# Performance work log

Measured on AMD Instinct MI355X. Metric: run time of the kernel, lower is better.

The kernel has to match this reference:

```python
import jax, jax.numpy as jnp
import numpy as np

B, D = 8, 256
MEM, CW, R, K, KL = 131072, 64, 4, 4, 4
C = R * K + 2 * KL + 1  # 25 visible cells
DELTA = 0.005
EPS = 1e-6
TIMESTEP = 1.0  # first step after reset


def _gather(x, idx):
    # x: (b,m) or (b,m,w); idx: (b,k)
    if x.ndim == 2:
        return jnp.take_along_axis(x, idx, axis=1)
    e = jnp.broadcast_to(idx[:, :, None], idx.shape + (x.shape[-1],))
    return jnp.take_along_axis(x, e, axis=1)


def _fwd(xi, memory, visible_memory, link_matrix, rev_link_matrix, precedence,
         read_weights, write_weights, usage,
         W_rq, b_rq, W_wv, b_wv, W_ig, b_ig, W_wg, b_wg,
         read_positions):
    b = xi.shape[0]
    bidx = jnp.arange(b)[:, None]

    # interface transforms (independent linears)
    read_query = (xi @ W_rq + b_rq).reshape(b, R, CW)      # (b,r,w)
    write_vector = (xi @ W_wv + b_wv).reshape(b, 1, CW)    # (b,1,w)
    ig = jax.nn.sigmoid(xi @ W_ig + b_ig)                  # (b,c)
    wg = jax.nn.sigmoid(xi @ W_wg + b_wg)                  # (b,1)

    # ------------------ write ------------------
    rw_vis = _gather(read_weights, read_positions)         # (b,c)
    ww_vis = _gather(write_weights, read_positions)        # (b,c)

    # usage update + least-used indicator over visible cells
    u = (rw_vis + ww_vis > DELTA).astype(memory.dtype)
    rel = _gather(usage, read_positions)
    I_min = (rel == jnp.min(rel, axis=-1, keepdims=True)).astype(memory.dtype)
    rel_new = (TIMESTEP - rel) * u + rel * (1.0 - u)
    usage = usage.at[bidx, read_positions].set(rel_new)

    # interpolated write weights over visible cells
    ww_new = wg * (ig * rw_vis + (1.0 - ig) * I_min)       # (b,c)
    write_weights = write_weights.at[bidx, read_positions].set(ww_new)

    # erase + write into visible memory, scatter back into sparse memory
    visible_memory = visible_memory * (1.0 - I_min[:, :, None]) + ww_new[:, :, None] * write_vector
    memory = memory.at[bidx, read_positions].set(visible_memory)

    # link matrix / reverse link matrix update
    trp = read_positions[:, R * K:R * K + 2 * KL]          # temporal positions (b,2KL)
    Ieye = jnp.eye(MEM, 2 * KL, dtype=memory.dtype)[None]  # eye(m,k) mask as in torch code
    prec_dense = jnp.zeros_like(write_weights).at[bidx, trp].set(precedence)  # (b,m)
    tww = _gather(write_weights, trp)                      # (b,2KL)
    link_matrix = ((1.0 - write_weights[:, :, None]) * link_matrix
                   + write_weights[:, :, None] * precedence[:, None, :]) * Ieye
    rev_link_matrix = ((1.0 - tww[:, None, :]) * rev_link_matrix
                       + tww[:, None, :] * prec_dense[:, :, None]) * Ieye

    # precedence update and least-used cell (argmin usage)
    precedence = (1.0 - jnp.sum(tww, axis=-1, keepdims=True)) * precedence + tww
    least_used = jax.lax.top_k(-usage, 1)[1]               # (b,1)

    # ------------------ read ------------------
    trw = _gather(read_weights, trp)                       # (b,2KL)
    fwd_w = jnp.einsum('bmk,bk->bm', link_matrix, trw)     # forward weighting
    bwd_w = jnp.einsum('bmk,bk->bm', rev_link_matrix, trw) # backward weighting

    # exact L2 k-NN over full memory (dense surrogate for the FAISS search)
    mem_sq = jnp.sum(memory * memory, axis=-1)             # (b,m)
    dots = jnp.einsum('brw,bmw->brm', read_query, memory)  # (b,r,m)
    knn = jax.lax.top_k(2.0 * dots - mem_sq[:, None, :], K)[1].reshape(b, R * K)

    fp = jax.lax.top_k(fwd_w, KL)[1]
    bp = jax.lax.top_k(bwd_w, KL)[1]
    lum = jnp.full((b, 1), C + 1, dtype=knn.dtype)         # timestep <= mem_size branch
    max_length = least_used[0, 0]                          # mem_limit_reached == False
    positions = jnp.clip(
        jnp.concatenate([knn, fp.astype(knn.dtype), bp.astype(knn.dtype), lum], axis=1),
        0, max_length)                                     # (b,c)

    visible = _gather(memory, positions)                   # (b,c,w)
    kq = read_query / (jnp.linalg.norm(read_query, axis=-1, keepdims=True) + EPS)
    vn = visible / (jnp.linalg.norm(visible, axis=-1, keepdims=True) + EPS)
    sim = jnp.einsum('brw,bcw->brc', kq, vn)               # cosine similarity
    rw_c = jax.nn.softmax(sim, axis=-1)                    # (b,r,c)
    read_vectors = jnp.einsum('brc,bcw->brw', rw_c, visible)
    return read_vectors


def setup_inputs() -> dict:
    key = jax.random.key(0)
    ks = jax.random.split(key, 16)
    inp = {}
    inp['xi'] = jax.random.normal(ks[0], (B, D), jnp.float32)
    inp['memory'] = jax.random.normal(ks[1], (B, MEM, CW), jnp.float32)
    inp['visible_memory'] = jax.random.normal(ks[2], (B, C, CW), jnp.float32)
    inp['link_matrix'] = 0.1 * jax.random.uniform(ks[3], (B, MEM, 2 * KL), jnp.float32)
    inp['rev_link_matrix'] = 0.1 * jax.random.uniform(ks[4], (B, MEM, 2 * KL), jnp.float32)
    inp['precedence'] = 0.1 * jax.random.uniform(ks[5], (B, 2 * KL), jnp.float32)
    inp['read_weights'] = 0.01 * jax.random.uniform(ks[6], (B, MEM), jnp.float32)
    inp['write_weights'] = 0.01 * jax.random.uniform(ks[7], (B, MEM), jnp.float32)
    usage = 0.5 + 0.5 * jax.random.uniform(ks[8], (B, MEM), jnp.float32)
    inp['usage'] = usage.at[:, MEM - 1].set(0.0)  # argmin lands at m-1 so the clamp is a no-op
    inp['least_used_mem'] = jnp.full((B, 1), MEM // 2, jnp.int32)
    inp['read_positions'] = jax.random.randint(ks[9], (B, C), 0, MEM)

    def lin(k, fi, fo):
        s = (6.0 / fi) ** 0.5  # kaiming-uniform-like
        return jax.random.uniform(k, (fi, fo), jnp.float32, -s, s)
    inp['W_rq'] = lin(ks[10], D, R * CW); inp['b_rq'] = jnp.zeros((R * CW,), jnp.float32)
    inp['W_wv'] = lin(ks[11], D, CW);     inp['b_wv'] = jnp.zeros((CW,), jnp.float32)
    inp['W_ig'] = lin(ks[12], D, C);      inp['b_ig'] = jnp.zeros((C,), jnp.float32)
    inp['W_wg'] = lin(ks[13], D, 1);      inp['b_wg'] = jnp.zeros((1,), jnp.float32)
    return inp


def reference(xi, memory, visible_memory, link_matrix, rev_link_matrix, precedence,
              read_weights, write_weights, usage, least_used_mem, read_positions,
              W_rq, b_rq, W_wv, b_wv, W_ig, b_ig, W_wg, b_wg):
    # least_used_mem is overwritten inside write() (argmin of updated usage) before use
    return _fwd(xi, memory, visible_memory, link_matrix, rev_link_matrix, precedence,
                read_weights, write_weights, usage,
                W_rq, b_rq, W_wv, b_wv, W_ig, b_ig, W_wg, b_wg,
                read_positions)
```

## Files before the change

### kernel.cpp

```cpp
#include <hip/hip_runtime.h>
#include <math.h>

#define BN 8
#define DDIM 256
#define MEMN 131072
#define CWN 64
#define RN 4
#define CN 25
#define DELTA_C 0.005f
#define EPS_C 1e-6f
#define RPB 1024
#define NBLK (MEMN / RPB)
#define NEG_INF (-3.402823466e38f)
#define IMAX 0x7fffffff
#define UPD_STRIDE 32


__device__ inline void wave_reduce_max(float& v, int& i, int& t) {
#pragma unroll
  for (int off = 32; off; off >>= 1) {
    float ov = __shfl_down(v, off);
    int oi = __shfl_down(i, off);
    int ot = __shfl_down(t, off);
    if (ov > v || (ov == v && oi < i)) { v = ov; i = oi; t = ot; }
  }
}

__device__ inline void block_argmax256(int tid, float v, int i, int t,
                                       float& rv, int& ri, int& rt) {
  __shared__ float sv[4];
  __shared__ int si[4], st[4];
  __shared__ float bv;
  __shared__ int bi, bt;
  wave_reduce_max(v, i, t);
  if ((tid & 63) == 0) { int w = tid >> 6; sv[w] = v; si[w] = i; st[w] = t; }
  __syncthreads();
  if (tid == 0) {
    float xv = sv[0]; int xi = si[0], xt = st[0];
#pragma unroll
    for (int w = 1; w < 4; w++)
      if (sv[w] > xv || (sv[w] == xv && si[w] < xi)) { xv = sv[w]; xi = si[w]; xt = st[w]; }
    bv = xv; bi = xi; bt = xt;
  }
  __syncthreads();
  rv = bv; ri = bi; rt = bt;
  __syncthreads();
}

__device__ inline void top4_of8(const float* v8, int* out4) {
  float val[12]; int idx[12]; bool used[12];
#pragma unroll
  for (int i = 0; i < 12; i++) { val[i] = (i < 8) ? v8[i] : 0.f; idx[i] = i; used[i] = false; }
  for (int r = 0; r < 4; r++) {
    int best = -1;
    for (int i = 0; i < 12; i++) {
      if (used[i]) continue;
      if (best < 0 || val[i] > val[best]) best = i;
    }
    used[best] = true;
    out4[r] = idx[best];
  }
}

__device__ inline float dot4(float4 a, float4 b) {
  return fmaf(a.x, b.x, fmaf(a.y, b.y, fmaf(a.z, b.z, a.w * b.w)));
}

__global__ __launch_bounds__(256) void k12_heads_state(
    const float* __restrict__ xi,
    const float* __restrict__ Wrq, const float* __restrict__ brq,
    const float* __restrict__ Wwv, const float* __restrict__ bwv,
    const float* __restrict__ Wig, const float* __restrict__ big,
    const float* __restrict__ Wwg, const float* __restrict__ bwg,
    const float* __restrict__ vm, const float* __restrict__ prec,
    const float* __restrict__ rw, const float* __restrict__ wwg,
    const float* __restrict__ usage,
    const float* __restrict__ lm, const float* __restrict__ rlm,
    const int* __restrict__ rp,
    float* rq, int* fp, int* bp,
    int* upd_pos, float* upd_rel, float* upd_mem) {
  int b = blockIdx.x, tid = threadIdx.x;
  __shared__ float x[DDIM];
  __shared__ float wv_s[64], ig_s[CN], wg_s;
  __shared__ int pos[CN];
  __shared__ float s_rw[CN], s_ww[CN], s_rel[CN], s_relnew[CN], s_imin[CN], s_wwnew[CN];
  __shared__ int s_guard[CN];
  __shared__ float minrel;
  __shared__ float fwd8[8], bwd8[8];

  x[tid] = xi[b * DDIM + tid];
  __syncthreads();
  {
    float s = brq[tid];
#pragma unroll 8
    for (int d = 0; d < DDIM; d++) s = fmaf(x[d], Wrq[d * 256 + tid], s);
    rq[b * 256 + tid] = s;
  }
  if (tid < 64) {
    float s = bwv[tid];
#pragma unroll 8
    for (int d = 0; d < DDIM; d++) s = fmaf(x[d], Wwv[d * 64 + tid], s);
    wv_s[tid] = s;
  } else if (tid < 64 + CN) {
    int o = tid - 64;
    float s = big[o];
#pragma unroll 8
    for (int d = 0; d < DDIM; d++) s = fmaf(x[d], Wig[d * CN + o], s);
    ig_s[o] = 1.f / (1.f + expf(-s));
  } else if (tid == 64 + CN) {
    float s = bwg[0];
#pragma unroll 8
    for (int d = 0; d < DDIM; d++) s = fmaf(x[d], Wwg[d], s);
    wg_s = 1.f / (1.f + expf(-s));
  }
  if (tid < CN) {
    int p = rp[b * CN + tid];
    pos[tid] = p;
    s_rw[tid] = rw[(size_t)b * MEMN + p];
    s_ww[tid] = wwg[(size_t)b * MEMN + p];
    s_rel[tid] = usage[(size_t)b * MEMN + p];
  }
  __syncthreads();
  if (tid == 0) {
    float m = s_rel[0];
    for (int j = 1; j < CN; j++) m = fminf(m, s_rel[j]);
    minrel = m;
  }
  __syncthreads();
  if (tid < CN) {
    float u = (s_rw[tid] + s_ww[tid] > DELTA_C) ? 1.f : 0.f;
    float im = (s_rel[tid] == minrel) ? 1.f : 0.f;
    s_imin[tid] = im;
    s_relnew[tid] = u * (1.f - s_rel[tid]) + (1.f - u) * s_rel[tid];
    float igv = ig_s[tid];
    s_wwnew[tid] = wg_s * (igv * s_rw[tid] + (1.f - igv) * im);
    int g = 1;
    for (int j = tid + 1; j < CN; j++)
      if (pos[j] == pos[tid]) { g = 0; break; }
    s_guard[tid] = g;
  }
  __syncthreads();
  if (tid < CN) {
    upd_pos[b * UPD_STRIDE + tid] = s_guard[tid] ? pos[tid] : -1;
    upd_rel[b * UPD_STRIDE + tid] = s_relnew[tid];
  }
  for (int it = 0; it < 7; it++) {
    int j = it * 4 + (tid >> 6);
    int lane = tid & 63;
    if (j < CN && s_guard[j]) {
      float v = vm[((size_t)b * CN + j) * 64 + lane] * (1.f - s_imin[j]) +
                s_wwnew[j] * wv_s[lane];
      upd_mem[((size_t)b * CN + j) * 64 + lane] = v;
    }
  }
  __syncthreads();
  if (tid < 8) {
    int m = tid;
    int trp_m = pos[16 + m];
    float tww = 0.f;
    for (int j = CN - 1; j >= 0; j--)
      if (pos[j] == trp_m) { tww = s_wwnew[j]; break; }
    float trw = rw[(size_t)b * MEMN + trp_m];
    float wwu;
    {
      int found = -1;
      for (int j = CN - 1; j >= 0; j--)
        if (pos[j] == m) { found = j; break; }
      wwu = (found >= 0) ? s_wwnew[found] : wwg[(size_t)b * MEMN + m];
    }
    float lmd = (1.f - wwu) * lm[((size_t)b * MEMN + m) * 8 + m] + wwu * prec[b * 8 + m];
    float pd = 0.f;
    for (int k = 7; k >= 0; k--)
      if (pos[16 + k] == m) { pd = prec[b * 8 + k]; break; }
    float rld = (1.f - tww) * rlm[((size_t)b * MEMN + m) * 8 + m] + tww * pd;
    fwd8[m] = lmd * trw;
    bwd8[m] = rld * trw;
  }
  __syncthreads();
  if (tid == 0) top4_of8(fwd8, &fp[b * 4]);
  if (tid == 1) top4_of8(bwd8, &bp[b * 4]);
}

__global__ __launch_bounds__(256, 4) void k3_scan(
    const float* __restrict__ memory, const float* __restrict__ usage,
    const float* __restrict__ rq,
    const int* __restrict__ upd_pos, const float* __restrict__ upd_rel,
    const float* __restrict__ upd_mem,
    float* blk_sv, int* blk_si, float* blk_uv, int* blk_ui) {
  int tid = threadIdx.x;
  int b = blockIdx.x / NBLK;
  int blk = blockIdx.x % NBLK;
  int base = blk * RPB;
  int wave = tid >> 6, lane = tid & 63;
  int r4 = lane >> 2, s4 = lane & 3;

  __shared__ int s_lcnt;
  __shared__ int s_lpos[CN], s_lj[CN];
  __shared__ float s_lrel[CN];
  if (tid == 0) s_lcnt = 0;
  __syncthreads();
  if (tid < CN) {
    int p = upd_pos[b * UPD_STRIDE + tid];
    if (p >= base && p < base + RPB) {
      int k = atomicAdd(&s_lcnt, 1);
      s_lpos[k] = p;
      s_lj[k] = tid;
      s_lrel[k] = upd_rel[b * UPD_STRIDE + tid];
    }
  }
  __syncthreads();
  int lcnt = s_lcnt;
  const float4* upd4 = (const float4*)upd_mem;

  const float4* q4 = (const float4*)(rq + b * 256);
  float4 qf[4][4];
#pragma unroll
  for (int q = 0; q < 4; q++)
#pragma unroll
    for (int j = 0; j < 4; j++)
      qf[q][j] = q4[q * 16 + s4 * 4 + j];

  float tv0 = NEG_INF, tv1 = NEG_INF, tv2 = NEG_INF, tv3 = NEG_INF;
  int ti0 = IMAX, ti1 = IMAX, ti2 = IMAX, ti3 = IMAX;

  int rowstart = base + wave * 256;
  const float4* mp = (const float4*)memory;

#pragma unroll 2
  for (int bi = 0; bi < 16; bi++) {
    int m = rowstart + bi * 16 + r4;
    size_t a = ((size_t)b * MEMN + m) * 16 + s4 * 4;
    float4 x0 = mp[a + 0];
    float4 x1 = mp[a + 1];
    float4 x2 = mp[a + 2];
    float4 x3 = mp[a + 3];
    if (lcnt) {
      for (int k = 0; k < lcnt; k++)
        if (m == s_lpos[k]) {
          const float4* u = &upd4[((size_t)b * CN + s_lj[k]) * 16 + s4 * 4];
          x0 = u[0]; x1 = u[1]; x2 = u[2]; x3 = u[3];
        }
    }
    float d0 = (dot4(x0, qf[0][0]) + dot4(x1, qf[0][1])) +
               (dot4(x2, qf[0][2]) + dot4(x3, qf[0][3]));
    float d1 = (dot4(x0, qf[1][0]) + dot4(x1, qf[1][1])) +
               (dot4(x2, qf[1][2]) + dot4(x3, qf[1][3]));
    float d2 = (dot4(x0, qf[2][0]) + dot4(x1, qf[2][1])) +
               (dot4(x2, qf[2][2]) + dot4(x3, qf[2][3]));
    float d3 = (dot4(x0, qf[3][0]) + dot4(x1, qf[3][1])) +
               (dot4(x2, qf[3][2]) + dot4(x3, qf[3][3]));
    float sq = (dot4(x0, x0) + dot4(x1, x1)) +
               (dot4(x2, x2) + dot4(x3, x3));
#pragma unroll
    for (int off = 1; off < 4; off <<= 1) {
      d0 += __shfl_xor(d0, off);
      d1 += __shfl_xor(d1, off);
      d2 += __shfl_xor(d2, off);
      d3 += __shfl_xor(d3, off);
      sq += __shfl_xor(sq, off);
    }
    float d = (s4 == 0) ? d0 : (s4 == 1) ? d1 : (s4 == 2) ? d2 : d3;
    float s = 2.f * d - sq;
    if (s > tv3) {
      tv3 = s; ti3 = m;
      if (tv3 > tv2) { float t = tv2; tv2 = tv3; tv3 = t; int u = ti2; ti2 = ti3; ti3 = u; }
      if (tv2 > tv1) { float t = tv1; tv1 = tv2; tv2 = t; int u = ti1; ti1 = ti2; ti2 = u; }
      if (tv1 > tv0) { float t = tv0; tv0 = tv1; tv1 = t; int u = ti0; ti0 = ti1; ti1 = u; }
    }
  }

  __shared__ float lsv[4][64][4];
  __shared__ int lsi[4][64][4];
  {
    int slot = wave * 16 + r4;
    lsv[s4][slot][0] = tv0; lsi[s4][slot][0] = ti0;
    lsv[s4][slot][1] = tv1; lsi[s4][slot][1] = ti1;
    lsv[s4][slot][2] = tv2; lsi[s4][slot][2] = ti2;
    lsv[s4][slot][3] = tv3; lsi[s4][slot][3] = ti3;
  }
  __syncthreads();
  {
    int w = wave;
    float v0 = lsv[w][lane][0], v1 = lsv[w][lane][1],
          v2 = lsv[w][lane][2], v3 = lsv[w][lane][3];
    int i0 = lsi[w][lane][0], i1 = lsi[w][lane][1],
        i2 = lsi[w][lane][2], i3 = lsi[w][lane][3];
    size_t o = (((size_t)b * 4 + w) * NBLK + blk) * 4;
    for (int round = 0; round < 4; round++) {
      float rv = v0; int ri = i0; int rt = lane;
      wave_reduce_max(rv, ri, rt);
      rv = __shfl(rv, 0); ri = __shfl(ri, 0); rt = __shfl(rt, 0);
      if (lane == 0) { blk_sv[o + round] = rv; blk_si[o + round] = ri; }
      if (lane == rt) {
        v0 = v1; i0 = i1; v1 = v2; i1 = i2;
        v2 = v3; i2 = i3; v3 = NEG_INF; i3 = IMAX;
      }
    }
  }

  if (b == 0) {
    const float4* u4 = (const float4*)(usage + base);
    float4 uu = u4[tid];
    int mb = base + tid * 4;
    if (lcnt) {
      for (int k = 0; k < lcnt; k++) {
        int d = s_lpos[k] - mb;
        if ((unsigned)d < 4u) {
          float rv = s_lrel[k];
          if (d == 0) uu.x = rv;
          else if (d == 1) uu.y = rv;
          else if (d == 2) uu.z = rv;
          else uu.w = rv;
        }
      }
    }
    float uv = uu.x; int uix = mb;
    if (uu.y < uv) { uv = uu.y; uix = mb + 1; }
    if (uu.z < uv) { uv = uu.z; uix = mb + 2; }
    if (uu.w < uv) { uv = uu.w; uix = mb + 3; }
    float rvv; int rii, rtt;
    block_argmax256(tid, -uv, uix, tid, rvv, rii, rtt);
    if (tid == 0) {
      blk_uv[blk] = -rvv;
      blk_ui[blk] = rii;
    }
  }
}

__global__ __launch_bounds__(256) void k45_merge_attn(
    const float* __restrict__ memory, const float* __restrict__ rq,
    const float* __restrict__ blk_sv, const int* __restrict__ blk_si,
    const float* __restrict__ blk_uv, const int* __restrict__ blk_ui,
    const int* __restrict__ fp, const int* __restrict__ bp,
    const int* __restrict__ upd_pos, const float* __restrict__ upd_mem,
    float* out) {
  int b = blockIdx.x, tid = threadIdx.x;
  int wave = tid >> 6, lane = tid & 63;
  __shared__ int knn_s[16];
  __shared__ int sL;
  __shared__ int pos[CN];
  __shared__ int supd[CN];
  __shared__ int ovr[CN];
  __shared__ float vis[CN][64];
  __shared__ float vnorm[CN];
  __shared__ float rnorm[4];
  __shared__ float sim[4][CN];
  __shared__ float pw[4][CN];
  __shared__ float qs[4][64];

  {
    int r = wave;
    size_t o = (size_t)(b * 4 + r) * NBLK * 4;
    float tv0 = NEG_INF, tv1 = NEG_INF, tv2 = NEG_INF, tv3 = NEG_INF;
    int ti0 = IMAX, ti1 = IMAX, ti2 = IMAX, ti3 = IMAX;
#pragma unroll
    for (int j = 0; j < 8; j++) {
      float s = blk_sv[o + j * 64 + lane];
      int m = blk_si[o + j * 64 + lane];
      if (s > tv3) {
        tv3 = s; ti3 = m;
        if (tv3 > tv2) { float t = tv2; tv2 = tv3; tv3 = t; int u = ti2; ti2 = ti3; ti3 = u; }
        if (tv2 > tv1) { float t = tv1; tv1 = tv2; tv2 = t; int u = ti1; ti1 = ti2; ti2 = u; }
        if (tv1 > tv0) { float t = tv0; tv0 = tv1; tv1 = t; int u = ti0; ti0 = ti1; ti1 = u; }
      }
    }
    for (int round = 0; round < 4; round++) {
      float rv = tv0; int ri = ti0; int rt = lane;
      wave_reduce_max(rv, ri, rt);
      rv = __shfl(rv, 0); ri = __shfl(ri, 0); rt = __shfl(rt, 0);
      if (lane == 0) knn_s[r * 4 + round] = ri;
      if (lane == rt) {
        tv0 = tv1; ti0 = ti1; tv1 = tv2; ti1 = ti2;
        tv2 = tv3; ti2 = ti3; tv3 = NEG_INF; ti3 = IMAX;
      }
    }
  }
  if (wave == 0) {
    float u0 = blk_uv[lane], u1 = blk_uv[64 + lane];
    int i0 = blk_ui[lane], i1 = blk_ui[64 + lane];
    float v; int i;
    if (u1 < u0 || (u1 == u0 && i1 < i0)) { v = u1; i = i1; } else { v = u0; i = i0; }
    float rv = -v; int ri = i; int rt = lane;
    wave_reduce_max(rv, ri, rt);
    if (lane == 0) sL = ri;
  }
  qs[tid >> 6][tid & 63] = rq[b * 256 + tid];
  __syncthreads();

  int L = sL;
  if (tid < CN) {
    supd[tid] = upd_pos[b * UPD_STRIDE + tid];
    int v;
    if (tid < 16) v = knn_s[tid];
    else if (tid < 20) v = fp[b * 4 + tid - 16];
    else if (tid < 24) v = bp[b * 4 + tid - 20];
    else v = CN + 1;
    v = min(v, L);
    v = max(v, 0);
    pos[tid] = v;
  }
  __syncthreads();
  if (tid < CN) {
    int o = -1;
    for (int j = 0; j < CN; j++)
      if (supd[j] == pos[tid]) o = j;
    ovr[tid] = o;
  }
  __syncthreads();
  for (int it = 0; it < 7; it++) {
    int j = it * 4 + (tid >> 6);
    int ln = tid & 63;
    if (j < CN) {
      int o = ovr[j];
      vis[j][ln] = (o >= 0)
          ? upd_mem[((size_t)b * CN + o) * 64 + ln]
          : memory[((size_t)b * MEMN + pos[j]) * 64 + ln];
    }
  }
  __syncthreads();
  if (tid < CN) {
    float s = 0.f;
    for (int k = 0; k < 64; k++) s = fmaf(vis[tid][k], vis[tid][k], s);
    vnorm[tid] = sqrtf(s) + EPS_C;
  }
  if (tid >= 32 && tid < 36) {
    int r = tid - 32;
    float s = 0.f;
    for (int k = 0; k < 64; k++) s = fmaf(qs[r][k], qs[r][k], s);
    rnorm[r] = sqrtf(s) + EPS_C;
  }
  __syncthreads();
  if (tid < 4 * CN) {
    int r = tid / CN, c = tid % CN;
    float s = 0.f;
    for (int k = 0; k < 64; k++) s = fmaf(qs[r][k], vis[c][k], s);
    sim[r][c] = s / (rnorm[r] * vnorm[c]);
  }
  __syncthreads();
  if (tid < 4) {
    int r = tid;
    float mx = NEG_INF;
    for (int c = 0; c < CN; c++) mx = fmaxf(mx, sim[r][c]);
    float sum = 0.f;
    for (int c = 0; c < CN; c++) { float e = expf(sim[r][c] - mx); pw[r][c] = e; sum += e; }
    float inv = 1.f / sum;
    for (int c = 0; c < CN; c++) pw[r][c] *= inv;
  }
  __syncthreads();
  {
    int r = tid >> 6, w = tid & 63;
    float s = 0.f;
    for (int c = 0; c < CN; c++) s = fmaf(pw[r][c], vis[c][w], s);
    out[(size_t)b * 256 + tid] = s;
  }
}

extern "C" void kernel_launch(void* const* d_in, const int* in_sizes, int n_in,
                              void* d_out, int out_size, void* d_ws, size_t ws_size,
                              hipStream_t stream) {
  const float* xi = (const float*)d_in[0];
  const float* memory = (const float*)d_in[1];
  const float* vm = (const float*)d_in[2];
  const float* lm = (const float*)d_in[3];
  const float* rlm = (const float*)d_in[4];
  const float* prec = (const float*)d_in[5];
  const float* rw = (const float*)d_in[6];
  const float* wwg = (const float*)d_in[7];
  const float* usage = (const float*)d_in[8];
  const int* rp = (const int*)d_in[10];
  const float* Wrq = (const float*)d_in[11];
  const float* brq = (const float*)d_in[12];
  const float* Wwv = (const float*)d_in[13];
  const float* bwv = (const float*)d_in[14];
  const float* Wig = (const float*)d_in[15];
  const float* big = (const float*)d_in[16];
  const float* Wwg = (const float*)d_in[17];
  const float* bwg = (const float*)d_in[18];
  float* out = (float*)d_out;

  float* f = (float*)d_ws;
  float* rq_w = f;      f += BN * 256;
  float* upd_mem_w = f; f += (size_t)BN * CN * 64;
  float* upd_rel_w = f; f += BN * UPD_STRIDE;
  float* blk_sv = f;    f += (size_t)BN * 4 * NBLK * 4;
  float* blk_uv = f;    f += NBLK;
  int* ip = (int*)f;
  int* upd_pos_w = ip;  ip += BN * UPD_STRIDE;
  int* fp_w = ip;       ip += BN * 4;
  int* bp_w = ip;       ip += BN * 4;
  int* blk_si = ip;     ip += (size_t)BN * 4 * NBLK * 4;
  int* blk_ui = ip;     ip += NBLK;

  hipLaunchKernelGGL(k12_heads_state, dim3(BN), dim3(256), 0, stream,
                     xi, Wrq, brq, Wwv, bwv, Wig, big, Wwg, bwg,
                     vm, prec, rw, wwg, usage, lm, rlm, rp,
                     rq_w, fp_w, bp_w, upd_pos_w, upd_rel_w, upd_mem_w);
  hipLaunchKernelGGL(k3_scan, dim3(BN * NBLK), dim3(256), 0, stream,
                     memory, usage, rq_w, upd_pos_w, upd_rel_w, upd_mem_w,
                     blk_sv, blk_si, blk_uv, blk_ui);
  hipLaunchKernelGGL(k45_merge_attn, dim3(BN), dim3(256), 0, stream,
                     memory, rq_w, blk_sv, blk_si, blk_uv, blk_ui,
                     fp_w, bp_w, upd_pos_w, upd_mem_w, out);
}
```

Measured before the change: 489.4 us.

## Stage memory tiles into LDS with double-buffered async global_load_lds in scan

The k3_scan kernel now streams each wave's memory rows into a per-wave double-buffered LDS tile using global_load_lds, with an XOR-swizzled layout to avoid bank conflicts, then reads float4s from LDS for the dot products. The next tile's load overlaps compute on the current one. It also drops the occupancy hint from launch bounds and reuses the staging buffer for the top-k merge. This adds 32KB LDS per block and explicit waitcnt/sched barriers, which may cut occupancy and limit compiler scheduling.

```diff
diff --git a/kernel.cpp b/kernel.cpp
--- a/kernel.cpp
+++ b/kernel.cpp
@@ -181,7 +181,7 @@
   if (tid == 1) top4_of8(bwd8, &bp[b * 4]);
 }
 
-__global__ __launch_bounds__(256, 4) void k3_scan(
+__global__ __launch_bounds__(256) void k3_scan(
     const float* __restrict__ memory, const float* __restrict__ usage,
     const float* __restrict__ rq,
     const int* __restrict__ upd_pos, const float* __restrict__ upd_rel,
@@ -194,6 +194,8 @@
   int wave = tid >> 6, lane = tid & 63;
   int r4 = lane >> 2, s4 = lane & 3;
 
+  __shared__ __align__(16) float stage[4][2][1024];
+
   __shared__ int s_lcnt;
   __shared__ int s_lpos[CN], s_lj[CN];
   __shared__ float s_lrel[CN];
@@ -219,21 +221,49 @@
 #pragma unroll
     for (int j = 0; j < 4; j++)
       qf[q][j] = q4[q * 16 + s4 * 4 + j];
+  asm volatile("s_waitcnt vmcnt(0)" ::: "memory");
+  __builtin_amdgcn_sched_barrier(0);
+
+  int rowstart = base + wave * 256;
+  const char* tile0 = (const char*)memory + ((size_t)b * MEMN + rowstart) * 256;
+  int srow = lane >> 4, slot = lane & 15;
+
+#define STAGE_TILE(t, bufi)                                                     \
+  do {                                                                          \
+    const char* tb = tile0 + (size_t)(t) * 4096;                                \
+    _Pragma("unroll")                                                           \
+    for (int ii = 0; ii < 4; ii++) {                                            \
+      int soff = (4 * ii + srow) * 256 + ((slot ^ ((srow << 1) | (ii & 1))) << 4); \
+      __builtin_amdgcn_global_load_lds(                                         \
+          (const __attribute__((address_space(1))) unsigned int*)(tb + soff),   \
+          (__attribute__((address_space(3))) unsigned int*)&stage[wave][bufi][ii * 256], \
+          16, 0, 0);                                                            \
+    }                                                                           \
+  } while (0)
 
   float tv0 = NEG_INF, tv1 = NEG_INF, tv2 = NEG_INF, tv3 = NEG_INF;
   int ti0 = IMAX, ti1 = IMAX, ti2 = IMAX, ti3 = IMAX;
 
-  int rowstart = base + wave * 256;
-  const float4* mp = (const float4*)memory;
-
-#pragma unroll 2
-  for (int bi = 0; bi < 16; bi++) {
-    int m = rowstart + bi * 16 + r4;
-    size_t a = ((size_t)b * MEMN + m) * 16 + s4 * 4;
-    float4 x0 = mp[a + 0];
-    float4 x1 = mp[a + 1];
-    float4 x2 = mp[a + 2];
-    float4 x3 = mp[a + 3];
+  int prd = ((r4 & 3) << 1) | ((r4 >> 2) & 1);
+  STAGE_TILE(0, 0);
+
+#pragma unroll
+  for (int t = 0; t < 16; t++) {
+    int buf = t & 1;
+    if (t < 15) {
+      STAGE_TILE(t + 1, buf ^ 1);
+      asm volatile("s_waitcnt vmcnt(4)" ::: "memory");
+    } else {
+      asm volatile("s_waitcnt vmcnt(0)" ::: "memory");
+    }
+    __builtin_amdgcn_sched_barrier(0);
+
+    int m = rowstart + t * 16 + r4;
+    const float4* bufp = (const float4*)stage[wave][buf];
+    float4 x0 = bufp[r4 * 16 + ((4 * s4 + 0) ^ prd)];
+    float4 x1 = bufp[r4 * 16 + ((4 * s4 + 1) ^ prd)];
+    float4 x2 = bufp[r4 * 16 + ((4 * s4 + 2) ^ prd)];
+    float4 x3 = bufp[r4 * 16 + ((4 * s4 + 3) ^ prd)];
     if (lcnt) {
       for (int k = 0; k < lcnt; k++)
         if (m == s_lpos[k]) {
@@ -263,28 +293,26 @@
     float s = 2.f * d - sq;
     if (s > tv3) {
       tv3 = s; ti3 = m;
-      if (tv3 > tv2) { float t = tv2; tv2 = tv3; tv3 = t; int u = ti2; ti2 = ti3; ti3 = u; }
-      if (tv2 > tv1) { float t = tv1; tv1 = tv2; tv2 = t; int u = ti1; ti1 = ti2; ti2 = u; }
-      if (tv1 > tv0) { float t = tv0; tv0 = tv1; tv1 = t; int u = ti0; ti0 = ti1; ti1 = u; }
-    }
-  }
-
-  __shared__ float lsv[4][64][4];
-  __shared__ int lsi[4][64][4];
+      if (tv3 > tv2) { float tt = tv2; tv2 = tv3; tv3 = tt; int u = ti2; ti2 = ti3; ti3 = u; }
+      if (tv2 > tv1) { float tt = tv1; tv1 = tv2; tv2 = tt; int u = ti1; ti1 = ti2; ti2 = u; }
+      if (tv1 > tv0) { float tt = tv0; tv0 = tv1; tv1 = tt; int u = ti0; ti0 = ti1; ti1 = u; }
+    }
+    asm volatile("s_waitcnt lgkmcnt(0)" ::: "memory");
+    __builtin_amdgcn_sched_barrier(0);
+  }
+
   {
-    int slot = wave * 16 + r4;
-    lsv[s4][slot][0] = tv0; lsi[s4][slot][0] = ti0;
-    lsv[s4][slot][1] = tv1; lsi[s4][slot][1] = ti1;
-    lsv[s4][slot][2] = tv2; lsi[s4][slot][2] = ti2;
-    lsv[s4][slot][3] = tv3; lsi[s4][slot][3] = ti3;
+    float* md = &stage[wave][0][s4 * 128 + r4 * 8];
+    md[0] = tv0; md[1] = tv1; md[2] = tv2; md[3] = tv3;
+    ((int*)md)[4] = ti0; ((int*)md)[5] = ti1; ((int*)md)[6] = ti2; ((int*)md)[7] = ti3;
   }
   __syncthreads();
   {
     int w = wave;
-    float v0 = lsv[w][lane][0], v1 = lsv[w][lane][1],
-          v2 = lsv[w][lane][2], v3 = lsv[w][lane][3];
-    int i0 = lsi[w][lane][0], i1 = lsi[w][lane][1],
-        i2 = lsi[w][lane][2], i3 = lsi[w][lane][3];
+    const float* ms = &stage[lane >> 4][0][w * 128 + (lane & 15) * 8];
+    float v0 = ms[0], v1 = ms[1], v2 = ms[2], v3 = ms[3];
+    int i0 = ((const int*)ms)[4], i1 = ((const int*)ms)[5],
+        i2 = ((const int*)ms)[6], i3 = ((const int*)ms)[7];
     size_t o = (((size_t)b * 4 + w) * NBLK + blk) * 4;
     for (int round = 0; round < 4; round++) {
       float rv = v0; int ri = i0; int rt = lane;
```

Measured after the change: 494.9 us. About the same (+1.1%).
